# Kernel tuning notes

Hardware: AMD Instinct MI355X
Metric: run time of the kernel (lower is better)

The kernel has to match this reference:

```python
import jax, jax.numpy as jnp
import numpy as np

B, N, D = 4, 2048, 512
H, DH = 8, 64  # heads, dim_head; hidden = H*DH = 512


def setup_inputs() -> dict:
    key = jax.random.key(0)
    k1, k2, k3, k4 = jax.random.split(key, 4)
    x = jax.random.normal(k1, (B, N, D), dtype=jnp.float32)
    pos_bias = jax.random.normal(k2, (H, N, N), dtype=jnp.float32) * 0.02
    w_qkv = jax.random.normal(k3, (D, 3 * H * DH), dtype=jnp.float32) * 0.02
    w_out = jax.random.normal(k4, (H * DH, D), dtype=jnp.float32) * 0.02
    return {"x": x, "pos_bias": pos_bias, "w_qkv": w_qkv, "w_out": w_out}


def reference(x, pos_bias, w_qkv, w_out):
    scale = DH ** (-0.5)
    qkv = x @ w_qkv                                   # [B, N, 3*H*DH]
    q, k, v = jnp.split(qkv, 3, axis=-1)
    # '... n (h d) -> ... h n d'
    def split_heads(t):
        return t.reshape(B, N, H, DH).transpose(0, 2, 1, 3)  # [B, H, N, DH]
    q, k, v = split_heads(q), split_heads(k), split_heads(v)
    q = q * scale
    sim = jnp.einsum('bhid,bhjd->bhij', q, k)         # [B, H, N, N]
    sim = sim + pos_bias                              # broadcast over batch
    # original subtracts detached row-max then softmax; jax.nn.softmax does
    # the same stable (stop-gradient max-subtract) computation.
    attn = jax.nn.softmax(sim, axis=-1)
    out = jnp.einsum('bhij,bhjd->bhid', attn, v)      # [B, H, N, DH]
    out = out.transpose(0, 2, 1, 3).reshape(B, N, H * DH)
    return out @ w_out                                # [B, N, D]
```

## Files before the change

kernel.cpp:

```cpp
#include <hip/hip_runtime.h>

typedef short bf16x8 __attribute__((ext_vector_type(8)));
typedef float f32x4 __attribute__((ext_vector_type(4)));

#define MFMA16(a, b, c) __builtin_amdgcn_mfma_f32_16x16x32_bf16(a, b, c, 0, 0, 0)

__device__ __forceinline__ short f2bf(float f) {
  unsigned u = __builtin_bit_cast(unsigned, f);
  u += 0x7fffu + ((u >> 16) & 1u);
  return (short)(u >> 16);
}

__device__ __forceinline__ void gload16(const void* g, void* l) {
  __builtin_amdgcn_global_load_lds(
      (const __attribute__((address_space(1))) void*)g,
      (__attribute__((address_space(3))) void*)l, 16, 0, 0);
}

#define L2E 1.44269504088896f


__global__ __launch_bounds__(256) void cvt_bf16(const float* __restrict__ in,
                                                short* __restrict__ out) {
  size_t i = ((size_t)blockIdx.x * 256 + threadIdx.x) * 8;
  const float4* p = (const float4*)(in + i);
  float4 a = p[0], b = p[1];
  bf16x8 v;
  v[0] = f2bf(a.x); v[1] = f2bf(a.y); v[2] = f2bf(a.z); v[3] = f2bf(a.w);
  v[4] = f2bf(b.x); v[5] = f2bf(b.y); v[6] = f2bf(b.z); v[7] = f2bf(b.w);
  *(bf16x8*)(out + i) = v;
}

__global__ __launch_bounds__(256) void transpose_cvt(const float* __restrict__ in,
                                                     short* __restrict__ out,
                                                     int K, int N) {
  __shared__ short Ts[64][72];
  const int t = threadIdx.x;
  const int k0 = blockIdx.y * 64, n1 = blockIdx.x * 64;
  const int kk = t >> 2, nq = (t & 3) * 16;
  const float* src = in + (size_t)(k0 + kk) * N + n1 + nq;
#pragma unroll
  for (int i = 0; i < 16; ++i) Ts[nq + i][kk] = f2bf(src[i]);
  __syncthreads();
  const int n = t >> 2, kq = (t & 3) * 16;
  short* dst = out + (size_t)(n1 + n) * K + k0 + kq;
  *(bf16x8*)dst = *(const bf16x8*)&Ts[n][kq];
  *(bf16x8*)(dst + 8) = *(const bf16x8*)&Ts[n][kq + 8];
}


__device__ __forceinline__ void gemm128_async(const short* __restrict__ A,
                                              const short* __restrict__ BT,
                                              int m0, int n0,
                                              char* As, char* Bs,
                                              f32x4 acc[4][4]) {
  const int t = threadIdx.x;
  const int w = t >> 6, lane = t & 63, l15 = lane & 15, quad = lane >> 4;
  const int wm = (w & 1) * 64, wn = (w >> 1) * 64;
  const int scol = ((lane & 3) ^ ((lane >> 3) & 3)) << 4;
  const char* ag = (const char*)A + (size_t)(m0 + w * 32 + (lane >> 2)) * 1024 + scol;
  const char* bg = (const char*)BT + (size_t)(n0 + w * 32 + (lane >> 2)) * 1024 + scol;
  char* al = As + w * 2048;
  char* bl = Bs + w * 2048;
  const int rsw = (quad ^ ((l15 >> 1) & 3)) << 4;
  const int ra = (wm + l15) * 64 + rsw;
  const int rb = (wn + l15) * 64 + rsw;

#define GQ_STAGE(BUF, KB)                                                      \
  do {                                                                         \
    gload16(ag + (KB), al + (BUF) * 8192);                                     \
    gload16(ag + 16384 + (KB), al + (BUF) * 8192 + 1024);                      \
    gload16(bg + (KB), bl + (BUF) * 8192);                                     \
    gload16(bg + 16384 + (KB), bl + (BUF) * 8192 + 1024);                      \
  } while (0)

  GQ_STAGE(0, 0);
  __syncthreads();
#pragma unroll 2
  for (int s = 0; s < 16; ++s) {
    const int buf = s & 1;
    if (s < 15) GQ_STAGE(buf ^ 1, (s + 1) * 64);
    bf16x8 af[4], bfr[4];
#pragma unroll
    for (int i = 0; i < 4; ++i)
      af[i] = *(const bf16x8*)(As + buf * 8192 + ra + i * 1024);
#pragma unroll
    for (int j = 0; j < 4; ++j)
      bfr[j] = *(const bf16x8*)(Bs + buf * 8192 + rb + j * 1024);
#pragma unroll
    for (int i = 0; i < 4; ++i)
#pragma unroll
      for (int j = 0; j < 4; ++j)
        acc[i][j] = MFMA16(af[i], bfr[j], acc[i][j]);
    __syncthreads();
  }
#undef GQ_STAGE
}


__global__ __launch_bounds__(256) void gemm_qkv(const short* __restrict__ A,
                                                const short* __restrict__ BT,
                                                short* __restrict__ q_ws,
                                                short* __restrict__ k_ws,
                                                short* __restrict__ v_t) {
  __shared__ short As[2][128][32];
  __shared__ short Bs[2][128][32];
  __shared__ short Ts[64][136];
  const int t = threadIdx.x;
  const int w = t >> 6, lane = t & 63, l15 = lane & 15, quad = lane >> 4;
  const int wm = (w & 1) * 64, wn = (w >> 1) * 64;
  const int m0 = blockIdx.y * 128, n0 = blockIdx.x * 128;
  f32x4 acc[4][4];
#pragma unroll
  for (int i = 0; i < 4; ++i)
#pragma unroll
    for (int j = 0; j < 4; ++j) acc[i][j] = (f32x4){0.f, 0.f, 0.f, 0.f};

  gemm128_async(A, BT, m0, n0, (char*)&As[0][0][0], (char*)&Bs[0][0][0], acc);

  const int which = n0 >> 9;
  const int b = m0 >> 11, seq0 = m0 & 2047;
  if (which < 2) {
    short* dst = (which == 0) ? q_ws : k_ws;
    const float scale = (which == 0) ? (0.125f * L2E) : 1.0f;
#pragma unroll
    for (int i = 0; i < 4; ++i)
#pragma unroll
      for (int j = 0; j < 4; ++j)
#pragma unroll
        for (int r = 0; r < 4; ++r) {
          int m_loc = wm + i * 16 + quad * 4 + r;
          int col = n0 + wn + j * 16 + l15;
          int h = (col >> 6) & 7, d = col & 63;
          dst[((size_t)(b * 8 + h) * 2048 + seq0 + m_loc) * 64 + d] =
              f2bf(acc[i][j][r] * scale);
        }
  } else {
    for (int half = 0; half < 2; ++half) {
      __syncthreads();
      if ((w >> 1) == half) {
#pragma unroll
        for (int i = 0; i < 4; ++i)
#pragma unroll
          for (int j = 0; j < 4; ++j)
#pragma unroll
            for (int r = 0; r < 4; ++r)
              Ts[j * 16 + l15][wm + i * 16 + quad * 4 + r] = f2bf(acc[i][j][r]);
      }
      __syncthreads();
      const int hd = ((n0 + half * 64) >> 6) & 7;
      const int dp = t >> 2, sq = (t & 3) * 32;
      short* dstp = v_t + ((size_t)(b * 8 + hd) * 64 + dp) * 2048 + seq0 + sq;
#pragma unroll
      for (int u = 0; u < 4; ++u)
        *(bf16x8*)(dstp + u * 8) = *(const bf16x8*)&Ts[dp][sq + u * 8];
    }
  }
}


#define ATTN_STAGE(BUFD, J0N)                                                  \
  do {                                                                         \
    _Pragma("unroll") for (int i_ = 0; i_ < 2; ++i_) {                         \
      const int ch_ = w * 2 + i_;                                              \
      const int off_ = ch_ * 1024 + lane * 16;                                 \
      const int row_ = off_ >> 7;                                              \
      const int col_ = (off_ & 127) ^ ((row_ & 7) << 4);                       \
      const char* gk_ = (const char*)k_ws +                                    \
          ((size_t)bh * 2048 + (size_t)(J0N) + row_) * 128 + col_;             \
      const char* gv_ = (const char*)v_t +                                     \
          ((size_t)bh * 64 + row_) * 4096 + (size_t)(J0N) * 2 + col_;          \
      gload16(gk_, (char*)&Ks[BUFD][0][0] + ch_ * 1024);                       \
      gload16(gv_, (char*)&Vs[BUFD][0][0] + ch_ * 1024);                       \
    }                                                                          \
  } while (0)

#define ATTN_LOADB(BV, J0N)                                                    \
  do {                                                                         \
    _Pragma("unroll") for (int nt_ = 0; nt_ < 4; ++nt_)                        \
        _Pragma("unroll") for (int r_ = 0; r_ < 4; ++r_)                       \
            BV[nt_][r_] = brow[r_][(J0N) + nt_ * 16];                          \
  } while (0)

#define ATTN_BODY(BUFC, BVC, BVN, J0N, DONEXT)                                 \
  do {                                                                         \
    if (DONEXT) {                                                              \
      ATTN_STAGE((BUFC) ^ 1, (J0N));                                           \
      ATTN_LOADB(BVN, (J0N));                                                  \
    }                                                                          \
    f32x4 S_[4];                                                               \
    _Pragma("unroll") for (int nt_ = 0; nt_ < 4; ++nt_) {                      \
      const char* kb_ = (const char*)&Ks[BUFC][0][0] + (nt_ * 16 + l15) * 128; \
      bf16x8 k0_ = *(const bf16x8*)(kb_ + cs);                                 \
      bf16x8 k1_ = *(const bf16x8*)(kb_ + (cs ^ 64));                          \
      f32x4 s_ = (f32x4){0.f, 0.f, 0.f, 0.f};                                  \
      s_ = MFMA16(aQ0, k0_, s_);                                               \
      s_ = MFMA16(aQ1, k1_, s_);                                               \
      S_[nt_] = s_;                                                            \
    }                                                                          \
    _Pragma("unroll") for (int nt_ = 0; nt_ < 4; ++nt_) {                      \
      float p0_ = exp2f(fmaf(BVC[nt_][0], L2E, S_[nt_][0]));                   \
      float p1_ = exp2f(fmaf(BVC[nt_][1], L2E, S_[nt_][1]));                   \
      float p2_ = exp2f(fmaf(BVC[nt_][2], L2E, S_[nt_][2]));                   \
      float p3_ = exp2f(fmaf(BVC[nt_][3], L2E, S_[nt_][3]));                   \
      lsum[0] += p0_; lsum[1] += p1_; lsum[2] += p2_; lsum[3] += p3_;          \
      unsigned pk01_, pk23_;                                                   \
      asm("v_cvt_pk_bf16_f32 %0, %1, %2" : "=v"(pk01_) : "v"(p0_), "v"(p1_)); \
      asm("v_cvt_pk_bf16_f32 %0, %1, %2" : "=v"(pk23_) : "v"(p2_), "v"(p3_)); \
      char* pb_ = (char*)&Pw[w][0][0];                                         \
      const int c0_ = 2 * (nt_ * 16 + l15);                                    \
      const int q4_ = quad * 4;                                                \
      *(short*)(pb_ + (q4_ + 0) * 128 + (c0_ ^ (((q4_ + 0) & 7) << 4))) =      \
          (short)pk01_;                                                        \
      *(short*)(pb_ + (q4_ + 1) * 128 + (c0_ ^ (((q4_ + 1) & 7) << 4))) =      \
          (short)(pk01_ >> 16);                                                \
      *(short*)(pb_ + (q4_ + 2) * 128 + (c0_ ^ (((q4_ + 2) & 7) << 4))) =      \
          (short)pk23_;                                                        \
      *(short*)(pb_ + (q4_ + 3) * 128 + (c0_ ^ (((q4_ + 3) & 7) << 4))) =      \
          (short)(pk23_ >> 16);                                                \
    }                                                                          \
    {                                                                          \
      const char* pr_ = (const char*)&Pw[w][0][0] + l15 * 128;                 \
      bf16x8 aP0 = *(const bf16x8*)(pr_ + cs);                                 \
      bf16x8 aP1 = *(const bf16x8*)(pr_ + (cs ^ 64));                          \
      _Pragma("unroll") for (int dt_ = 0; dt_ < 4; ++dt_) {                    \
        const char* vb_ =                                                      \
            (const char*)&Vs[BUFC][0][0] + (dt_ * 16 + l15) * 128;             \
        bf16x8 v0_ = *(const bf16x8*)(vb_ + cs);                               \
        bf16x8 v1_ = *(const bf16x8*)(vb_ + (cs ^ 64));                        \
        O[dt_] = MFMA16(aP0, v0_, O[dt_]);                                     \
        O[dt_] = MFMA16(aP1, v1_, O[dt_]);                                     \
      }                                                                        \
    }                                                                          \
    __builtin_amdgcn_sched_barrier(0);                                         \
    asm volatile("s_waitcnt vmcnt(16)" ::: "memory");                          \
    __builtin_amdgcn_s_barrier();                                              \
    __builtin_amdgcn_sched_barrier(0);                                         \
  } while (0)

__global__ __launch_bounds__(256)
__attribute__((amdgpu_waves_per_eu(4, 4)))
void attn_kernel(const short* __restrict__ q_ws,
                 const short* __restrict__ k_ws,
                 const short* __restrict__ v_t,
                 const float* __restrict__ bias,
                 short* __restrict__ attnO) {
  __shared__ short Ks[2][64][64];
  __shared__ short Vs[2][64][64];
  __shared__ short Pw[4][16][64];
  const int t = threadIdx.x;
  const int w = t >> 6, lane = t & 63, l15 = lane & 15, quad = lane >> 4;
  const int bid = blockIdx.x;
  const int h = bid & 7;
  const int b = (bid >> 3) & 3;
  const int qb = bid >> 5;
  const int bh = b * 8 + h;
  const int q0 = qb * 64 + w * 16;
  const int cs = (quad * 16) ^ ((l15 & 7) << 4);

  const size_t qbase = ((size_t)bh * 2048 + q0 + l15) * 64 + quad * 8;
  bf16x8 aQ0 = *(const bf16x8*)(q_ws + qbase);
  bf16x8 aQ1 = *(const bf16x8*)(q_ws + qbase + 32);

  f32x4 O[4];
#pragma unroll
  for (int i = 0; i < 4; ++i) O[i] = (f32x4){0.f, 0.f, 0.f, 0.f};
  float lsum[4] = {0.f, 0.f, 0.f, 0.f};

  const float* brow[4];
#pragma unroll
  for (int r = 0; r < 4; ++r)
    brow[r] = bias + ((size_t)h * 2048 + q0 + quad * 4 + r) * 2048 + l15;

  float bvA[4][4], bvB[4][4];
  ATTN_STAGE(0, 0);
  ATTN_LOADB(bvA, 0);
  __syncthreads();

  for (int it = 0; it < 16; ++it) {
    const int j0 = it * 128;
    ATTN_BODY(0, bvA, bvB, j0 + 64, 1);
    ATTN_BODY(1, bvB, bvA, j0 + 128, (it < 15));
  }

#pragma unroll
  for (int off = 1; off <= 8; off <<= 1)
#pragma unroll
    for (int r = 0; r < 4; ++r) lsum[r] += __shfl_xor(lsum[r], off);
#pragma unroll
  for (int r = 0; r < 4; ++r) lsum[r] = 1.f / lsum[r];
#pragma unroll
  for (int dt = 0; dt < 4; ++dt)
#pragma unroll
    for (int r = 0; r < 4; ++r) {
      size_t row = (size_t)b * 2048 + q0 + quad * 4 + r;
      attnO[row * 512 + h * 64 + dt * 16 + l15] = f2bf(O[dt][r] * lsum[r]);
    }
#undef ATTN_STAGE
#undef ATTN_LOADB
#undef ATTN_BODY
}


__global__ __launch_bounds__(256) void gemm_out(const short* __restrict__ A,
                                                const short* __restrict__ BT,
                                                float* __restrict__ out) {
  __shared__ short As[2][128][32];
  __shared__ short Bs[2][128][32];
  const int t = threadIdx.x;
  const int w = t >> 6, lane = t & 63, l15 = lane & 15, quad = lane >> 4;
  const int wm = (w & 1) * 64, wn = (w >> 1) * 64;
  const int m0 = blockIdx.y * 128, n0 = blockIdx.x * 128;
  f32x4 acc[4][4];
#pragma unroll
  for (int i = 0; i < 4; ++i)
#pragma unroll
    for (int j = 0; j < 4; ++j) acc[i][j] = (f32x4){0.f, 0.f, 0.f, 0.f};

  gemm128_async(A, BT, m0, n0, (char*)&As[0][0][0], (char*)&Bs[0][0][0], acc);

#pragma unroll
  for (int i = 0; i < 4; ++i)
#pragma unroll
    for (int j = 0; j < 4; ++j)
#pragma unroll
      for (int r = 0; r < 4; ++r)
        out[(size_t)(m0 + wm + i * 16 + quad * 4 + r) * 512 + n0 + wn + j * 16 + l15] =
            acc[i][j][r];
}


extern "C" void kernel_launch(void* const* d_in, const int* in_sizes, int n_in,
                              void* d_out, int out_size, void* d_ws, size_t ws_size,
                              hipStream_t stream) {
  (void)in_sizes; (void)n_in; (void)out_size; (void)ws_size;
  const float* x        = (const float*)d_in[0];
  const float* pos_bias = (const float*)d_in[1];
  const float* w_qkv    = (const float*)d_in[2];
  const float* w_out    = (const float*)d_in[3];
  float* out = (float*)d_out;

  short* ws = (short*)d_ws;
  const size_t SEG = (size_t)32 * 2048 * 64;
  short* q_ws  = ws;
  short* k_ws  = q_ws + SEG;
  short* v_t   = k_ws + SEG;
  short* attnO = v_t + SEG;
  short* xbf   = attnO + SEG;
  short* wqkvT = xbf + SEG;
  short* woutT = wqkvT + (size_t)1536 * 512;

  cvt_bf16<<<2048, 256, 0, stream>>>(x, xbf);
  transpose_cvt<<<dim3(24, 8), 256, 0, stream>>>(w_qkv, wqkvT, 512, 1536);
  transpose_cvt<<<dim3(8, 8), 256, 0, stream>>>(w_out, woutT, 512, 512);
  gemm_qkv<<<dim3(12, 64), 256, 0, stream>>>(xbf, wqkvT, q_ws, k_ws, v_t);
  attn_kernel<<<1024, 256, 0, stream>>>(q_ws, k_ws, v_t, pos_bias, attnO);
  gemm_out<<<dim3(4, 64), 256, 0, stream>>>(attnO, woutT, out);
}
```

Before: 360.2 us.

## Merge prep kernels, stage Q/K stores through LDS, add MFMA priority hints

Three conversion and transpose launches are merged into one prep kernel, which removes two launch overheads. The Q/K epilogue of the QKV GEMM now stages results in shared memory and writes 16-byte coalesced rows, replacing scattered 2-byte global stores. The attention loop raises wave priority around its MFMA sections with s_setprio so matrix work gets issue preference over other waves. The costs are two extra block barriers in the GEMM epilogue and a possible scheduling effect from the priority hints.

```diff
diff --git a/kernel.cpp b/kernel.cpp
--- a/kernel.cpp
+++ b/kernel.cpp
@@ -20,23 +20,11 @@
 #define L2E 1.44269504088896f
 
 
-__global__ __launch_bounds__(256) void cvt_bf16(const float* __restrict__ in,
-                                                short* __restrict__ out) {
-  size_t i = ((size_t)blockIdx.x * 256 + threadIdx.x) * 8;
-  const float4* p = (const float4*)(in + i);
-  float4 a = p[0], b = p[1];
-  bf16x8 v;
-  v[0] = f2bf(a.x); v[1] = f2bf(a.y); v[2] = f2bf(a.z); v[3] = f2bf(a.w);
-  v[4] = f2bf(b.x); v[5] = f2bf(b.y); v[6] = f2bf(b.z); v[7] = f2bf(b.w);
-  *(bf16x8*)(out + i) = v;
-}
-
-__global__ __launch_bounds__(256) void transpose_cvt(const float* __restrict__ in,
-                                                     short* __restrict__ out,
-                                                     int K, int N) {
-  __shared__ short Ts[64][72];
-  const int t = threadIdx.x;
-  const int k0 = blockIdx.y * 64, n1 = blockIdx.x * 64;
+__device__ __forceinline__ void transpose_body(const float* __restrict__ in,
+                                               short* __restrict__ out,
+                                               int K, int N, int bx, int by,
+                                               short (*Ts)[72], int t) {
+  const int k0 = by * 64, n1 = bx * 64;
   const int kk = t >> 2, nq = (t & 3) * 16;
   const float* src = in + (size_t)(k0 + kk) * N + n1 + nq;
 #pragma unroll
@@ -46,6 +34,31 @@
   short* dst = out + (size_t)(n1 + n) * K + k0 + kq;
   *(bf16x8*)dst = *(const bf16x8*)&Ts[n][kq];
   *(bf16x8*)(dst + 8) = *(const bf16x8*)&Ts[n][kq + 8];
+}
+
+__global__ __launch_bounds__(256) void prep(const float* __restrict__ x,
+                                            const float* __restrict__ w_qkv,
+                                            const float* __restrict__ w_out,
+                                            short* __restrict__ xbf,
+                                            short* __restrict__ wqkvT,
+                                            short* __restrict__ woutT) {
+  __shared__ short Ts[64][72];
+  const int bid = blockIdx.x, t = threadIdx.x;
+  if (bid < 2048) {
+    size_t i = ((size_t)bid * 256 + t) * 8;
+    const float4* p = (const float4*)(x + i);
+    float4 a = p[0], b = p[1];
+    bf16x8 v;
+    v[0] = f2bf(a.x); v[1] = f2bf(a.y); v[2] = f2bf(a.z); v[3] = f2bf(a.w);
+    v[4] = f2bf(b.x); v[5] = f2bf(b.y); v[6] = f2bf(b.z); v[7] = f2bf(b.w);
+    *(bf16x8*)(xbf + i) = v;
+  } else if (bid < 2240) {
+    const int sub = bid - 2048;
+    transpose_body(w_qkv, wqkvT, 512, 1536, sub % 24, sub / 24, Ts, t);
+  } else {
+    const int sub = bid - 2240;
+    transpose_body(w_out, woutT, 512, 512, sub % 8, sub / 8, Ts, t);
+  }
 }
 
 
@@ -123,18 +136,29 @@
   if (which < 2) {
     short* dst = (which == 0) ? q_ws : k_ws;
     const float scale = (which == 0) ? (0.125f * L2E) : 1.0f;
-#pragma unroll
-    for (int i = 0; i < 4; ++i)
-#pragma unroll
-      for (int j = 0; j < 4; ++j)
-#pragma unroll
-        for (int r = 0; r < 4; ++r) {
-          int m_loc = wm + i * 16 + quad * 4 + r;
-          int col = n0 + wn + j * 16 + l15;
-          int h = (col >> 6) & 7, d = col & 63;
-          dst[((size_t)(b * 8 + h) * 2048 + seq0 + m_loc) * 64 + d] =
-              f2bf(acc[i][j][r] * scale);
-        }
+    const int hA = (n0 >> 6) & 7;
+    for (int half = 0; half < 2; ++half) {
+      __syncthreads();
+      if ((w & 1) == half) {
+#pragma unroll
+        for (int i = 0; i < 4; ++i)
+#pragma unroll
+          for (int j = 0; j < 4; ++j)
+#pragma unroll
+            for (int r = 0; r < 4; ++r)
+              Ts[i * 16 + quad * 4 + r][wn + j * 16 + l15] =
+                  f2bf(acc[i][j][r] * scale);
+      }
+      __syncthreads();
+      const int ro = t >> 2, cg = t & 3;
+      short* dstp = dst +
+          ((size_t)(b * 8 + hA + (cg >> 1)) * 2048 + seq0 + half * 64 + ro) * 64 +
+          (cg & 1) * 32;
+      const short* srcp = &Ts[ro][cg * 32];
+#pragma unroll
+      for (int u = 0; u < 4; ++u)
+        *(bf16x8*)(dstp + u * 8) = *(const bf16x8*)(srcp + u * 8);
+    }
   } else {
     for (int half = 0; half < 2; ++half) {
       __syncthreads();
@@ -189,6 +213,7 @@
       ATTN_LOADB(BVN, (J0N));                                                  \
     }                                                                          \
     f32x4 S_[4];                                                               \
+    __builtin_amdgcn_s_setprio(1);                                             \
     _Pragma("unroll") for (int nt_ = 0; nt_ < 4; ++nt_) {                      \
       const char* kb_ = (const char*)&Ks[BUFC][0][0] + (nt_ * 16 + l15) * 128; \
       bf16x8 k0_ = *(const bf16x8*)(kb_ + cs);                                 \
@@ -198,6 +223,7 @@
       s_ = MFMA16(aQ1, k1_, s_);                                               \
       S_[nt_] = s_;                                                            \
     }                                                                          \
+    __builtin_amdgcn_s_setprio(0);                                             \
     _Pragma("unroll") for (int nt_ = 0; nt_ < 4; ++nt_) {                      \
       float p0_ = exp2f(fmaf(BVC[nt_][0], L2E, S_[nt_][0]));                   \
       float p1_ = exp2f(fmaf(BVC[nt_][1], L2E, S_[nt_][1]));                   \
@@ -223,6 +249,7 @@
       const char* pr_ = (const char*)&Pw[w][0][0] + l15 * 128;                 \
       bf16x8 aP0 = *(const bf16x8*)(pr_ + cs);                                 \
       bf16x8 aP1 = *(const bf16x8*)(pr_ + (cs ^ 64));                          \
+      __builtin_amdgcn_s_setprio(1);                                           \
       _Pragma("unroll") for (int dt_ = 0; dt_ < 4; ++dt_) {                    \
         const char* vb_ =                                                      \
             (const char*)&Vs[BUFC][0][0] + (dt_ * 16 + l15) * 128;             \
@@ -231,6 +258,7 @@
         O[dt_] = MFMA16(aP0, v0_, O[dt_]);                                     \
         O[dt_] = MFMA16(aP1, v1_, O[dt_]);                                     \
       }                                                                        \
+      __builtin_amdgcn_s_setprio(0);                                           \
     }                                                                          \
     __builtin_amdgcn_sched_barrier(0);                                         \
     asm volatile("s_waitcnt vmcnt(16)" ::: "memory");                          \
@@ -350,9 +378,7 @@
   short* wqkvT = xbf + SEG;
   short* woutT = wqkvT + (size_t)1536 * 512;
 
-  cvt_bf16<<<2048, 256, 0, stream>>>(x, xbf);
-  transpose_cvt<<<dim3(24, 8), 256, 0, stream>>>(w_qkv, wqkvT, 512, 1536);
-  transpose_cvt<<<dim3(8, 8), 256, 0, stream>>>(w_out, woutT, 512, 512);
+  prep<<<2304, 256, 0, stream>>>(x, w_qkv, w_out, xbf, wqkvT, woutT);
   gemm_qkv<<<dim3(12, 64), 256, 0, stream>>>(xbf, wqkvT, q_ws, k_ws, v_t);
   attn_kernel<<<1024, 256, 0, stream>>>(q_ws, k_ws, v_t, pos_bias, attnO);
   gemm_out<<<dim3(4, 64), 256, 0, stream>>>(attnO, woutT, out);
```

Result: slower. 380.2 us (+5.6%).
